# Kernel tuning notes

Hardware: AMD Instinct MI355X
Metric: run time of the kernel (lower is better)

Reference implementation:

```python
import jax, jax.numpy as jnp
import numpy as np

DN = ('NCHW', 'OIHW', 'NCHW')

def conv2d(x, w, b):
    y = jax.lax.conv_general_dilated(x, w, window_strides=(1, 1), padding='SAME', dimension_numbers=DN)
    return y + b[None, :, None, None]

def setup_inputs() -> dict:
    key = jax.random.key(0)
    ks = jax.random.split(key, 8)
    C = 256
    Cq = C // 8
    B, H, W = 8, 56, 56
    fan_out_qk = Cq * 9
    fan_out_v = C * 9
    std_qk = np.sqrt(2.0 / fan_out_qk)  # kaiming_normal fan_out, relu
    std_v = np.sqrt(2.0 / fan_out_v)
    return {
        'x': jax.random.normal(ks[0], (B, C, H, W), dtype=jnp.float32),
        'wq': jax.random.normal(ks[1], (Cq, C, 3, 3), dtype=jnp.float32) * std_qk,
        'bq': jnp.zeros((Cq,), dtype=jnp.float32),
        'wk': jax.random.normal(ks[2], (Cq, C, 3, 3), dtype=jnp.float32) * std_qk,
        'bk': jnp.zeros((Cq,), dtype=jnp.float32),
        'wv': jax.random.normal(ks[3], (C, C, 3, 3), dtype=jnp.float32) * std_v,
        'bv': jnp.zeros((C,), dtype=jnp.float32),
        'gamma': jax.random.uniform(ks[4], (1,), dtype=jnp.float32) * 0.1,
    }

def reference(x, wq, bq, wk, bk, wv, bv, gamma):
    B, C, H, W = x.shape
    N = H * W
    q = conv2d(x, wq, bq).reshape(B, -1, N)   # [B, C/8, N]
    k = conv2d(x, wk, bk).reshape(B, -1, N)   # [B, C/8, N]
    v = conv2d(x, wv, bv).reshape(B, C, N)    # [B, C, N]
    # energy[b,i,j] = sum_d q[b,d,i] * k[b,d,j]  (unscaled)
    energy = jnp.einsum('bdi,bdj->bij', q, k)
    attention = jax.nn.softmax(energy, axis=-1)  # [B, N, N]
    # out[b,c,i] = sum_j v[b,c,j] * attention[b,i,j]
    out = jnp.einsum('bcj,bij->bci', v, attention).reshape(B, C, H, W)
    return gamma[0] * out + x
```

## Files before the change

### kernel.cpp

```cpp
#include <hip/hip_runtime.h>
#include <math.h>

#define B_ 8
#define C_ 256
#define H_ 56
#define W_ 56
#define N_ 3136
#define BN_ (B_*N_)
#define LOG2E 1.44269504088896340736f

typedef __attribute__((ext_vector_type(8))) short short8;
typedef __attribute__((ext_vector_type(4))) float f32x4;
typedef __attribute__((ext_vector_type(16))) float f32x16;
typedef __attribute__((ext_vector_type(4))) unsigned short u16x4;
#define MFMA16(A, Bf, Cf) __builtin_amdgcn_mfma_f32_16x16x32_bf16((A), (Bf), (Cf), 0, 0, 0)
#define MFMA32(A, Bf, Cf) __builtin_amdgcn_mfma_f32_32x32x16_bf16((A), (Bf), (Cf), 0, 0, 0)

#define XT_ELEMS (B_*58*64*256)
#define A_ELEMS  (320*2304)
#define AHI_OFF  (2*XT_ELEMS)
#define ALO_OFF  (AHI_OFF + A_ELEMS)
#define QKT_HI_OFF (ALO_OFF + A_ELEMS)
#define QKT_ELEMS  (B_*N_*64)
#define QKT_LO_OFF (QKT_HI_OFF + QKT_ELEMS)
#define VBF_OFF    (QKT_LO_OFF + QKT_ELEMS)
#define VBF_ELEMS  (B_*C_*N_)

#define QF_ELEMS (B_*196*64*8)


#define SX(col) ((((col) & 3)) ^ (((col) >> 2) & 3))
#define SWZ(r, col, c8) ((((r)*64 + (col))*4) + ((c8) ^ SX(col)))

#define PSTR 76
#define VSTR 58

__device__ inline unsigned short f2bf(float f) {
    unsigned u = __float_as_uint(f);
    unsigned r = (u + 0x7fffu + ((u >> 16) & 1u)) >> 16;
    return (unsigned short)r;
}
__device__ inline float bf2f(unsigned short h) {
    return __uint_as_float(((unsigned)h) << 16);
}
__device__ inline float exp2_hw(float x) {
    float r; asm("v_exp_f32 %0, %1" : "=v"(r) : "v"(x)); return r;
}
__device__ inline unsigned cvt_pk_bf16(float lo, float hi) {
    unsigned r; asm("v_cvt_pk_bf16_f32 %0, %1, %2" : "=v"(r) : "v"(lo), "v"(hi)); return r;
}
__device__ inline void gl_lds16(const unsigned short* g, uint4* l) {
    __builtin_amdgcn_global_load_lds(
        (const __attribute__((address_space(1))) unsigned int*)g,
        (__attribute__((address_space(3))) unsigned int*)l,
        16, 0, 0);
}

__global__ __launch_bounds__(256) void zero_pads(
    unsigned short* __restrict__ xhi, unsigned short* __restrict__ xlo)
{
    const int g = blockIdx.x*256 + threadIdx.x;
    const int half = 61440;
    unsigned short* base = (g < half) ? xhi : xlo;
    const int i = (g < half) ? g : g - half;
    const int b = i / 7680, rem = i - b*7680;
    const int slot = rem >> 5, c8 = rem & 31;
    int row, col;
    if (slot < 64)       { row = 0;  col = slot; }
    else if (slot < 128) { row = 57; col = slot - 64; }
    else if (slot < 184) { row = slot - 127; col = 0; }
    else                 { row = slot - 183; col = 57; }
    const size_t o = ((size_t)((b*58 + row)*64 + col))*256 + c8*8;
    *(uint4*)(base + o) = make_uint4(0, 0, 0, 0);
}

__global__ __launch_bounds__(256) void prep_x(
    const float* __restrict__ x,
    unsigned short* __restrict__ xhi, unsigned short* __restrict__ xlo)
{
    __shared__ float xs[64][57];
    const int cc = blockIdx.x, y = blockIdx.y, b = blockIdx.z;
    const int t = threadIdx.x;
    const int c0 = cc * 64;
    for (int idx = t; idx < 64 * 56; idx += 256) {
        const int ch = idx / 56, xc = idx - ch * 56;
        xs[ch][xc] = x[((size_t)(b*C_ + c0 + ch)*H_ + y)*W_ + xc];
    }
    __syncthreads();
    for (int idx = t; idx < 56 * 32; idx += 256) {
        const int xc = idx >> 5, chp = idx & 31;
        const float v0 = xs[2*chp][xc], v1 = xs[2*chp + 1][xc];
        const unsigned short h0 = f2bf(v0), h1 = f2bf(v1);
        const unsigned short l0 = f2bf(v0 - bf2f(h0));
        const unsigned short l1 = f2bf(v1 - bf2f(h1));
        const size_t o = ((size_t)(b*58 + y + 1) * 64 + (xc + 1)) * 256 + c0 + 2*chp;
        *(unsigned*)(xhi + o) = (unsigned)h0 | ((unsigned)h1 << 16);
        *(unsigned*)(xlo + o) = (unsigned)l0 | ((unsigned)l1 << 16);
    }
}

__global__ __launch_bounds__(256) void prep_w(
    const float* __restrict__ wq, const float* __restrict__ wk,
    const float* __restrict__ wv,
    unsigned short* __restrict__ Ahi, unsigned short* __restrict__ Alo)
{
    const int g = blockIdx.x * 256 + threadIdx.x;
    if (g >= 320 * 2304) return;
    const int m = g / 2304, k = g - m * 2304;
    const int s = k >> 8, c = k & 255;
    float w;
    if (m < 32)      w = wq[((size_t)m*C_ + c)*9 + s];
    else if (m < 64) w = wk[((size_t)(m-32)*C_ + c)*9 + s];
    else             w = wv[((size_t)(m-64)*C_ + c)*9 + s];
    const unsigned short h = f2bf(w);
    const int cc = (k >> 5) & 7, quad = (k >> 3) & 3, e = k & 7;
    const size_t o = ((((size_t)(m >> 4)*9 + s)*8 + cc)*64 + (quad*16 + (m & 15)))*8 + e;
    Ahi[o] = h;
    Alo[o] = f2bf(w - bf2f(h));
}

__global__ __launch_bounds__(256, 3) void conv_fused(
    const unsigned short* __restrict__ xhi, const unsigned short* __restrict__ xlo,
    const unsigned short* __restrict__ Ahi, const unsigned short* __restrict__ Alo,
    const float* __restrict__ bq, const float* __restrict__ bk,
    const float* __restrict__ bv,
    unsigned short* __restrict__ qkt_hi, unsigned short* __restrict__ qkt_lo,
    unsigned short* __restrict__ vbf)
{
    __shared__ uint4 SMEM[3080];
    const int b = blockIdx.x, y = blockIdx.y, z = blockIdx.z;
    const int t = threadIdx.x;
    const int w = t >> 6, L = t & 63;
    const int ln = L & 15, quad = L >> 4;

    size_t gofs[3];
#pragma unroll
    for (int i = 0; i < 3; i++) {
        const int ci = w*192 + i*64 + L;
        const int r = ci >> 8, col = (ci >> 2) & 63;
        const int c8 = (ci & 3) ^ SX(col);
        gofs[i] = ((size_t)((b*58 + y + r)*64 + col))*256 + c8*8;
    }

    if (z == 0) {
        const int wrg = w >> 1, wnt = w & 1;
        f32x4 acc[2][2];
#pragma unroll
        for (int i = 0; i < 2; i++) { acc[i][0] = (f32x4)0.0f; acc[i][1] = (f32x4)0.0f; }

#pragma unroll
        for (int i = 0; i < 3; i++) {
            gl_lds16(xhi + gofs[i], SMEM + w*192 + i*64);
            gl_lds16(xlo + gofs[i], SMEM + 768 + w*192 + i*64);
        }
        __syncthreads();

        for (int cc = 0; cc < 8; cc++) {
            const int buf = cc & 1;
            const uint4* sH = SMEM + buf*1536;
            const uint4* sL = sH + 768;
            if (cc < 7) {
                uint4* nB = SMEM + (buf^1)*1536;
#pragma unroll
                for (int i = 0; i < 3; i++) {
                    gl_lds16(xhi + gofs[i] + (cc+1)*32, nB + w*192 + i*64);
                    gl_lds16(xlo + gofs[i] + (cc+1)*32, nB + 768 + w*192 + i*64);
                }
            }
#pragma unroll
            for (int s = 0; s < 9; s++) {
                const int dx = s % 3 - 1;
                const int r = s / 3;
                short8 ah[2], al[2];
#pragma unroll
                for (int rgi = 0; rgi < 2; rgi++) {
                    const int rg = wrg*2 + rgi;
                    const size_t aoff = (((size_t)(rg*9 + s)*8 + cc)*64 + L)*8;
                    ah[rgi] = *(const short8*)(Ahi + aoff);
                    al[rgi] = *(const short8*)(Alo + aoff);
                }
#pragma unroll
                for (int nti = 0; nti < 2; nti++) {
                    const int col = (wnt*2 + nti)*16 + ln + dx + 1;
                    const int i4 = SWZ(r, col, quad);
                    const short8 bh = *(const short8*)&sH[i4];
                    const short8 bl = *(const short8*)&sL[i4];
#pragma unroll
                    for (int rgi = 0; rgi < 2; rgi++) {
                        acc[rgi][nti] = MFMA16(ah[rgi], bh, acc[rgi][nti]);
                        acc[rgi][nti] = MFMA16(ah[rgi], bl, acc[rgi][nti]);
                        acc[rgi][nti] = MFMA16(al[rgi], bh, acc[rgi][nti]);
                    }
                }
            }
            if (cc < 7) __syncthreads();
        }

#pragma unroll
        for (int rgi = 0; rgi < 2; rgi++) {
            const int rg = wrg*2 + rgi;
            const int m0 = rg*16 + quad*4;
#pragma unroll
            for (int nti = 0; nti < 2; nti++) {
                const int px = (wnt*2 + nti)*16 + ln;
                if (px >= 56) continue;
                const int pix = y*56 + px;
                u16x4 hi4, lo4;
#pragma unroll
                for (int r = 0; r < 4; r++) {
                    const int m = m0 + r;
                    const float bias = (m < 32) ? bq[m] : bk[m - 32];
                    float val = acc[rgi][nti][r] + bias;
                    if (rg < 2) val *= LOG2E;
                    const unsigned short h = f2bf(val);
                    hi4[r] = h;
                    lo4[r] = f2bf(val - bf2f(h));
                }
                size_t o;
                if (rg < 2) {
                    o = ((size_t)(b*196 + (pix >> 4))*64 + (m0 >> 3)*16 + (pix & 15))*8 + (m0 & 7);
                } else {
                    const int mk0 = m0 - 32;
                    o = (size_t)QF_ELEMS +
                        (((size_t)(b*49 + (pix >> 6))*4 + ((pix >> 4) & 3))*64
                         + (mk0 >> 3)*16 + (pix & 15))*8 + (mk0 & 7);
                }
                *(u16x4*)(qkt_hi + o) = hi4;
                *(u16x4*)(qkt_lo + o) = lo4;
            }
        }
    } else {
        f32x4 acc[4][4];
#pragma unroll
        for (int rg = 0; rg < 4; rg++)
#pragma unroll
            for (int nt = 0; nt < 4; nt++) acc[rg][nt] = (f32x4)0.0f;

#pragma unroll
        for (int i = 0; i < 3; i++)
            gl_lds16(xhi + gofs[i], SMEM + w*192 + i*64);
        __syncthreads();

        for (int cc = 0; cc < 8; cc++) {
            const int buf = cc & 1;
            const uint4* sH = SMEM + buf*768;
            if (cc < 7) {
                uint4* nB = SMEM + (buf^1)*768;
#pragma unroll
                for (int i = 0; i < 3; i++)
                    gl_lds16(xhi + gofs[i] + (cc+1)*32, nB + w*192 + i*64);
            }
#pragma unroll
            for (int s = 0; s < 9; s++) {
                const int dx = s % 3 - 1;
                const int r = s / 3;
                short8 a[4];
#pragma unroll
                for (int rg = 0; rg < 4; rg++) {
                    const size_t aoff = (((size_t)((4 + w*4 + rg)*9 + s)*8 + cc)*64 + L)*8;
                    a[rg] = *(const short8*)(Ahi + aoff);
                }
#pragma unroll
                for (int nt = 0; nt < 4; nt++) {
                    const int col = nt*16 + ln + dx + 1;
                    const short8 bf = *(const short8*)&sH[SWZ(r, col, quad)];
#pragma unroll
                    for (int rg = 0; rg < 4; rg++)
                        acc[rg][nt] = MFMA16(a[rg], bf, acc[rg][nt]);
                }
            }
            __syncthreads();
        }

        unsigned short* Vs = (unsigned short*)SMEM;
#pragma unroll
        for (int rg = 0; rg < 4; rg++)
#pragma unroll
            for (int nt = 0; nt < 4; nt++) {
                const int px = nt*16 + ln;
                if (px >= 56) continue;
#pragma unroll
                for (int r = 0; r < 4; r++) {
                    const int cl = (w*4 + rg)*16 + quad*4 + r;
                    Vs[cl*VSTR + px] = f2bf(acc[rg][nt][r] + bv[cl]);
                }
            }
        __syncthreads();
        const int p0 = y*56;
        const int hh = L >> 5, c31 = L & 31;
        const int gend = (p0 + 55) >> 4;
        for (int gi = p0 >> 4; gi <= gend; gi++) {
            const int pxl0 = gi*16 + hh*8 - p0;
            if (pxl0 >= 0 && pxl0 + 8 <= 56) {
#pragma unroll
                for (int cgk = 0; cgk < 2; cgk++) {
                    const int cg = w*2 + cgk;
                    const short8 vv = *(const short8*)&Vs[(cg*32 + c31)*VSTR + pxl0];
                    const size_t o = ((((size_t)(b*8 + cg)*49 + (gi >> 2))*4 + (gi & 3))*64 + L)*8;
                    *(short8*)(vbf + o) = vv;
                }
            }
        }
    }
}

__global__ __launch_bounds__(128, 4) void attn_flash2w(
    const unsigned short* __restrict__ qkt_hi, const unsigned short* __restrict__ qkt_lo,
    const unsigned short* __restrict__ vbf,
    unsigned short* __restrict__ op0, unsigned short* __restrict__ op1,
    float* __restrict__ mlbase)
{
    __shared__ unsigned short P[2][32*PSTR];
    __shared__ float alphaL[2][32];

    const int bx = blockIdx.x;
    const int b = bx & 7, it = bx >> 3;
    const int chalf = blockIdx.y;
    const int jh = blockIdx.z;
    const int jt0 = jh * 25, njt = 25 - jh;
    const int i_base = it * 32;
    const int t = threadIdx.x;
    const int w = t >> 6, L = t & 63;
    const int ln = L & 15, quad = L >> 4;
    const int l32 = L & 31, h32 = L >> 5;

    const unsigned short* Kf_hi = qkt_hi + QF_ELEMS;
    const unsigned short* Kf_lo = qkt_lo + QF_ELEMS;

    const size_t qoff = ((size_t)(b*196 + it*2 + w)*64 + L)*8;
    const short8 qh = *(const short8*)(qkt_hi + qoff);
    const short8 ql = *(const short8*)(qkt_lo + qoff);

    float m_run = -INFINITY, l_run = 0.0f;
    f32x16 O0 = (f32x16)0.0f, O1 = (f32x16)0.0f;
    const int cg0 = chalf*4 + w*2;
    const unsigned short* vt0 = vbf + ((size_t)(b*8 + cg0)*49)*2048 + (size_t)L*8;
    const unsigned short* vt1 = vbf + ((size_t)(b*8 + cg0 + 1)*49)*2048 + (size_t)L*8;
    const unsigned short* kbh = Kf_hi + (size_t)b*49*2048 + (size_t)L*8;
    const unsigned short* kbl = Kf_lo + (size_t)b*49*2048 + (size_t)L*8;

    for (int jtl = 0; jtl < njt; jtl++) {
        const int jt = jt0 + jtl;
        const int buf = jtl & 1;

        short8 Va[4], Vb[4];
#pragma unroll
        for (int s = 0; s < 4; s++) {
            Va[s] = *(const short8*)(vt0 + jt*2048 + s*512);
            Vb[s] = *(const short8*)(vt1 + jt*2048 + s*512);
        }

        f32x4 sacc[4];
#pragma unroll
        for (int tj = 0; tj < 4; tj++) {
            const short8 kh = *(const short8*)(kbh + jt*2048 + tj*512);
            const short8 kl = *(const short8*)(kbl + jt*2048 + tj*512);
            f32x4 a = (f32x4)0.0f;
            a = MFMA16(kh, qh, a);
            a = MFMA16(kh, ql, a);
            a = MFMA16(kl, qh, a);
            sacc[tj] = a;
        }
        float mt0 = fmaxf(fmaxf(sacc[0][0], sacc[0][1]), fmaxf(sacc[0][2], sacc[0][3]));
        float mt1 = fmaxf(fmaxf(sacc[1][0], sacc[1][1]), fmaxf(sacc[1][2], sacc[1][3]));
        float mt2 = fmaxf(fmaxf(sacc[2][0], sacc[2][1]), fmaxf(sacc[2][2], sacc[2][3]));
        float mt3 = fmaxf(fmaxf(sacc[3][0], sacc[3][1]), fmaxf(sacc[3][2], sacc[3][3]));
        float mx = fmaxf(fmaxf(mt0, mt1), fmaxf(mt2, mt3));
        mx = fmaxf(mx, __shfl_xor(mx, 16));
        mx = fmaxf(mx, __shfl_xor(mx, 32));

        float alpha = 1.0f;
        if (__any(mx > m_run + 8.0f)) {
            const float m_new = fmaxf(m_run, mx);
            alpha = exp2_hw(m_run - m_new);
            m_run = m_new;
        }

#pragma unroll
        for (int tj = 0; tj < 4; tj++)
#pragma unroll
            for (int r = 0; r < 4; r++)
                sacc[tj][r] = exp2_hw(sacc[tj][r] - m_run);
        float s0 = (sacc[0][0] + sacc[0][1]) + (sacc[0][2] + sacc[0][3]);
        float s1 = (sacc[1][0] + sacc[1][1]) + (sacc[1][2] + sacc[1][3]);
        float s2 = (sacc[2][0] + sacc[2][1]) + (sacc[2][2] + sacc[2][3]);
        float s3 = (sacc[3][0] + sacc[3][1]) + (sacc[3][2] + sacc[3][3]);
        float ps = (s0 + s1) + (s2 + s3);
        ps += __shfl_xor(ps, 16);
        ps += __shfl_xor(ps, 32);
        l_run = l_run * alpha + ps;

        {
            unsigned short* prow = &P[buf][(w*16 + ln)*PSTR];
#pragma unroll
            for (int tj = 0; tj < 4; tj++) {
                uint2 pp;
                pp.x = cvt_pk_bf16(sacc[tj][0], sacc[tj][1]);
                pp.y = cvt_pk_bf16(sacc[tj][2], sacc[tj][3]);
                *(uint2*)(prow + tj*16 + quad*4) = pp;
            }
        }
        if (quad == 0) alphaL[buf][w*16 + ln] = alpha;

        __syncthreads();

        const float a = alphaL[buf][l32];
        if (__any(a != 1.0f)) {
#pragma unroll
            for (int rg = 0; rg < 16; rg++) { O0[rg] *= a; O1[rg] *= a; }
        }
        short8 Bp[4];
#pragma unroll
        for (int s = 0; s < 4; s++) {
            Bp[s] = *(const short8*)&P[buf][l32*PSTR + s*16 + h32*8];
            O0 = MFMA32(Va[s], Bp[s], O0);
        }
#pragma unroll
        for (int s = 0; s < 4; s++)
            O1 = MFMA32(Vb[s], Bp[s], O1);
    }

    if (chalf == 0 && quad == 0) {
        const int i = i_base + w*16 + ln;
        mlbase[jh*BN_ + b*N_ + i]       = m_run;
        mlbase[(2 + jh)*BN_ + b*N_ + i] = l_run;
    }
    unsigned short* OP = jh ? op1 : op0;
    const int pix = i_base + l32;
#pragma unroll
    for (int g = 0; g < 2; g++) {
        const f32x16 Ot = g ? O1 : O0;
        const int cg = chalf*128 + w*64 + g*32;
#pragma unroll
        for (int reg = 0; reg < 16; reg++) {
            const int c = cg + (reg & 3) + 8*(reg >> 2) + 4*h32;
            OP[(size_t)(b*C_ + c)*N_ + pix] = f2bf(Ot[reg]);
        }
    }
}

__global__ __launch_bounds__(256) void coef_pre(
    const float* __restrict__ mlbase, const float* __restrict__ gptr,
    float* __restrict__ coef)
{
    const int i = blockIdx.x*256 + threadIdx.x;
    const float m0 = mlbase[i],        m1 = mlbase[BN_ + i];
    const float l0 = mlbase[2*BN_ + i], l1 = mlbase[3*BN_ + i];
    const float mm = fmaxf(m0, m1);
    const float a0 = exp2_hw(m0 - mm), a1 = exp2_hw(m1 - mm);
    const float inv = gptr[0] / (a0*l0 + a1*l1);
    coef[2*i]   = a0 * inv;
    coef[2*i+1] = a1 * inv;
}

__global__ __launch_bounds__(256) void combine(
    const unsigned short* __restrict__ op0, const unsigned short* __restrict__ op1,
    const float* __restrict__ coef,
    const float* __restrict__ x, float* __restrict__ out)
{
    const int bc = blockIdx.x;
    const int b = bc >> 8;
    const size_t base = (size_t)bc * N_;
    const float2* cf = (const float2*)coef + (size_t)b * N_;
    for (int pq = threadIdx.x; pq < 784; pq += 256) {
        const int p0 = pq * 4;
        const ushort4 o0 = *(const ushort4*)(op0 + base + p0);
        const ushort4 o1 = *(const ushort4*)(op1 + base + p0);
        const float4 xx = *(const float4*)(x + base + p0);
        float4 r;
        { const float2 c = cf[p0 + 0]; r.x = xx.x + c.x*bf2f(o0.x) + c.y*bf2f(o1.x); }
        { const float2 c = cf[p0 + 1]; r.y = xx.y + c.x*bf2f(o0.y) + c.y*bf2f(o1.y); }
        { const float2 c = cf[p0 + 2]; r.z = xx.z + c.x*bf2f(o0.z) + c.y*bf2f(o1.z); }
        { const float2 c = cf[p0 + 3]; r.w = xx.w + c.x*bf2f(o0.w) + c.y*bf2f(o1.w); }
        *(float4*)(out + base + p0) = r;
    }
}

extern "C" void kernel_launch(void* const* d_in, const int* in_sizes, int n_in,
                              void* d_out, int out_size, void* d_ws, size_t ws_size,
                              hipStream_t stream)
{
    (void)in_sizes; (void)n_in; (void)out_size; (void)ws_size;
    const float* x  = (const float*)d_in[0];
    const float* wq = (const float*)d_in[1];
    const float* bq = (const float*)d_in[2];
    const float* wk = (const float*)d_in[3];
    const float* bk = (const float*)d_in[4];
    const float* wv = (const float*)d_in[5];
    const float* bv = (const float*)d_in[6];
    const float* gm = (const float*)d_in[7];
    float* out = (float*)d_out;

    unsigned short* u = (unsigned short*)d_ws;
    unsigned short* xhi = u;
    unsigned short* xlo = u + XT_ELEMS;
    unsigned short* Ahi = u + AHI_OFF;
    unsigned short* Alo = u + ALO_OFF;
    unsigned short* qkt_hi = u + QKT_HI_OFF;
    unsigned short* qkt_lo = u + QKT_LO_OFF;
    unsigned short* vbf = u + VBF_OFF;
    float* mlbase = (float*)Ahi;
    float* coef = (float*)Alo;

    hipLaunchKernelGGL(zero_pads, dim3(480), dim3(256), 0, stream, xhi, xlo);
    hipLaunchKernelGGL(prep_x, dim3(4, 56, 8), dim3(256), 0, stream, x, xhi, xlo);
    hipLaunchKernelGGL(prep_w, dim3(2880), dim3(256), 0, stream, wq, wk, wv, Ahi, Alo);
    hipLaunchKernelGGL(conv_fused, dim3(8, 56, 2), dim3(256), 0, stream,
                       xhi, xlo, Ahi, Alo, bq, bk, bv, qkt_hi, qkt_lo, vbf);
    hipLaunchKernelGGL(attn_flash2w, dim3(98*8, 2, 2), dim3(128), 0, stream,
                       qkt_hi, qkt_lo, vbf, xhi, xlo, mlbase);
    hipLaunchKernelGGL(coef_pre, dim3(98), dim3(256), 0, stream, mlbase, gm, coef);
    hipLaunchKernelGGL(combine, dim3(2048), dim3(256), 0, stream,
                       xhi, xlo, coef, x, out);
}
```

Baseline: 307.0 us.

## Drop key split in attention and fuse normalization and residual epilogue

```diff
diff --git a/kernel.cpp b/kernel.cpp
--- a/kernel.cpp
+++ b/kernel.cpp
@@ -307,17 +307,16 @@
 __global__ __launch_bounds__(128, 4) void attn_flash2w(
     const unsigned short* __restrict__ qkt_hi, const unsigned short* __restrict__ qkt_lo,
     const unsigned short* __restrict__ vbf,
-    unsigned short* __restrict__ op0, unsigned short* __restrict__ op1,
-    float* __restrict__ mlbase)
+    const float* __restrict__ x, const float* __restrict__ gptr,
+    float* __restrict__ out)
 {
     __shared__ unsigned short P[2][32*PSTR];
     __shared__ float alphaL[2][32];
+    __shared__ float lL[32];
 
     const int bx = blockIdx.x;
     const int b = bx & 7, it = bx >> 3;
     const int chalf = blockIdx.y;
-    const int jh = blockIdx.z;
-    const int jt0 = jh * 25, njt = 25 - jh;
     const int i_base = it * 32;
     const int t = threadIdx.x;
     const int w = t >> 6, L = t & 63;
@@ -335,13 +334,12 @@
     f32x16 O0 = (f32x16)0.0f, O1 = (f32x16)0.0f;
     const int cg0 = chalf*4 + w*2;
     const unsigned short* vt0 = vbf + ((size_t)(b*8 + cg0)*49)*2048 + (size_t)L*8;
-    const unsigned short* vt1 = vbf + ((size_t)(b*8 + cg0 + 1)*49)*2048 + (size_t)L*8;
+    const unsigned short* vt1 = vt0 + (size_t)49*2048;
     const unsigned short* kbh = Kf_hi + (size_t)b*49*2048 + (size_t)L*8;
     const unsigned short* kbl = Kf_lo + (size_t)b*49*2048 + (size_t)L*8;
 
-    for (int jtl = 0; jtl < njt; jtl++) {
-        const int jt = jt0 + jtl;
-        const int buf = jtl & 1;
+    for (int jt = 0; jt < 49; jt++) {
+        const int buf = jt & 1;
 
         short8 Va[4], Vb[4];
 #pragma unroll
@@ -420,12 +418,11 @@
             O1 = MFMA32(Vb[s], Bp[s], O1);
     }
 
-    if (chalf == 0 && quad == 0) {
-        const int i = i_base + w*16 + ln;
-        mlbase[jh*BN_ + b*N_ + i]       = m_run;
-        mlbase[(2 + jh)*BN_ + b*N_ + i] = l_run;
-    }
-    unsigned short* OP = jh ? op1 : op0;
+    __syncthreads();
+    if (quad == 0) lL[w*16 + ln] = l_run;
+    __syncthreads();
+    const float inv = gptr[0] / lL[l32];
+
     const int pix = i_base + l32;
 #pragma unroll
     for (int g = 0; g < 2; g++) {
@@ -434,45 +431,9 @@
 #pragma unroll
         for (int reg = 0; reg < 16; reg++) {
             const int c = cg + (reg & 3) + 8*(reg >> 2) + 4*h32;
-            OP[(size_t)(b*C_ + c)*N_ + pix] = f2bf(Ot[reg]);
-        }
-    }
-}
-
-__global__ __launch_bounds__(256) void coef_pre(
-    const float* __restrict__ mlbase, const float* __restrict__ gptr,
-    float* __restrict__ coef)
-{
-    const int i = blockIdx.x*256 + threadIdx.x;
-    const float m0 = mlbase[i],        m1 = mlbase[BN_ + i];
-    const float l0 = mlbase[2*BN_ + i], l1 = mlbase[3*BN_ + i];
-    const float mm = fmaxf(m0, m1);
-    const float a0 = exp2_hw(m0 - mm), a1 = exp2_hw(m1 - mm);
-    const float inv = gptr[0] / (a0*l0 + a1*l1);
-    coef[2*i]   = a0 * inv;
-    coef[2*i+1] = a1 * inv;
-}
-
-__global__ __launch_bounds__(256) void combine(
-    const unsigned short* __restrict__ op0, const unsigned short* __restrict__ op1,
-    const float* __restrict__ coef,
-    const float* __restrict__ x, float* __restrict__ out)
-{
-    const int bc = blockIdx.x;
-    const int b = bc >> 8;
-    const size_t base = (size_t)bc * N_;
-    const float2* cf = (const float2*)coef + (size_t)b * N_;
-    for (int pq = threadIdx.x; pq < 784; pq += 256) {
-        const int p0 = pq * 4;
-        const ushort4 o0 = *(const ushort4*)(op0 + base + p0);
-        const ushort4 o1 = *(const ushort4*)(op1 + base + p0);
-        const float4 xx = *(const float4*)(x + base + p0);
-        float4 r;
-        { const float2 c = cf[p0 + 0]; r.x = xx.x + c.x*bf2f(o0.x) + c.y*bf2f(o1.x); }
-        { const float2 c = cf[p0 + 1]; r.y = xx.y + c.x*bf2f(o0.y) + c.y*bf2f(o1.y); }
-        { const float2 c = cf[p0 + 2]; r.z = xx.z + c.x*bf2f(o0.z) + c.y*bf2f(o1.z); }
-        { const float2 c = cf[p0 + 3]; r.w = xx.w + c.x*bf2f(o0.w) + c.y*bf2f(o1.w); }
-        *(float4*)(out + base + p0) = r;
+            const size_t idx = (size_t)(b*C_ + c)*N_ + pix;
+            out[idx] = x[idx] + inv * Ot[reg];
+        }
     }
 }
 
@@ -499,17 +460,12 @@
     unsigned short* qkt_hi = u + QKT_HI_OFF;
     unsigned short* qkt_lo = u + QKT_LO_OFF;
     unsigned short* vbf = u + VBF_OFF;
-    float* mlbase = (float*)Ahi;
-    float* coef = (float*)Alo;
 
     hipLaunchKernelGGL(zero_pads, dim3(480), dim3(256), 0, stream, xhi, xlo);
     hipLaunchKernelGGL(prep_x, dim3(4, 56, 8), dim3(256), 0, stream, x, xhi, xlo);
     hipLaunchKernelGGL(prep_w, dim3(2880), dim3(256), 0, stream, wq, wk, wv, Ahi, Alo);
     hipLaunchKernelGGL(conv_fused, dim3(8, 56, 2), dim3(256), 0, stream,
                        xhi, xlo, Ahi, Alo, bq, bk, bv, qkt_hi, qkt_lo, vbf);
-    hipLaunchKernelGGL(attn_flash2w, dim3(98*8, 2, 2), dim3(128), 0, stream,
-                       qkt_hi, qkt_lo, vbf, xhi, xlo, mlbase);
-    hipLaunchKernelGGL(coef_pre, dim3(98), dim3(256), 0, stream, mlbase, gm, coef);
-    hipLaunchKernelGGL(combine, dim3(2048), dim3(256), 0, stream,
-                       xhi, xlo, coef, x, out);
-}
+    hipLaunchKernelGGL(attn_flash2w, dim3(98*8, 2), dim3(128), 0, stream,
+                       qkt_hi, qkt_lo, vbf, x, gm, out);
+}
```

New measurement: 295.5 us. 3.8% less time.
